# Kernel optimization log

Measured on AMD Instinct MI355X. Metric: run time of the kernel, lower is better.

## Reference

```python
import jax, jax.numpy as jnp
import numpy as np

N = 200000
E = 3200000
EPS = 1e-5


def setup_inputs() -> dict:
    key = jax.random.key(0)
    ks = jax.random.split(key, 8)
    x = jax.random.normal(ks[0], (N, 128), dtype=jnp.float32)
    edge_index = jax.random.randint(ks[1], (2, E), 0, N, dtype=jnp.int32)
    def lin(k, fi, fo):
        s = 1.0 / np.sqrt(fi)
        return jax.random.uniform(k, (fi, fo), jnp.float32, -s, s)
    return {
        "x": x,
        "edge_index": edge_index,
        "W1": lin(ks[2], 128, 256), "b1": jnp.zeros((256,), jnp.float32),
        "gamma1": jnp.ones((256,), jnp.float32), "beta1": jnp.zeros((256,), jnp.float32),
        "W2": lin(ks[3], 256, 256), "b2": jnp.zeros((256,), jnp.float32),
        "gamma2": jnp.ones((256,), jnp.float32), "beta2": jnp.zeros((256,), jnp.float32),
        "W3": lin(ks[4], 256, 40), "b3": jnp.zeros((40,), jnp.float32),
    }


def _gcn_norm(edge_index):
    # add self-loops, compute symmetric GCN normalization
    loop = jnp.arange(N, dtype=jnp.int32)
    row = jnp.concatenate([edge_index[0], loop])
    col = jnp.concatenate([edge_index[1], loop])
    deg = jax.ops.segment_sum(jnp.ones_like(row, dtype=jnp.float32), row, num_segments=N)
    dinv = jax.lax.rsqrt(jnp.maximum(deg, 1.0))  # deg >= 1 due to self-loops
    norm = dinv[row] * dinv[col]  # [E+N]
    return row, col, norm


def _gcn_conv(x, W, b, row, col, norm):
    h = x @ W                                  # [N, Fout] small GEMM
    msg = h[col] * norm[:, None]               # gather + scale  [E+N, Fout]
    out = jax.ops.segment_sum(msg, row, num_segments=N)  # scatter-add
    return out + b


def _batchnorm(x, gamma, beta):
    mu = jnp.mean(x, axis=0)
    var = jnp.var(x, axis=0)
    return (x - mu) * jax.lax.rsqrt(var + EPS) * gamma + beta


def reference(x, edge_index, W1, b1, gamma1, beta1, W2, b2, gamma2, beta2, W3, b3):
    row, col, norm = _gcn_norm(edge_index)
    h = _gcn_conv(x, W1, b1, row, col, norm)
    h = jax.nn.relu(_batchnorm(h, gamma1, beta1))
    h = _gcn_conv(h, W2, b2, row, col, norm)
    h = jax.nn.relu(_batchnorm(h, gamma2, beta2))
    h = _gcn_conv(h, W3, b3, row, col, norm)
    return jax.nn.log_softmax(h, axis=-1)
```

## Files before the change

kernel.cpp:

```cpp
#include <hip/hip_runtime.h>
#include <hip/hip_bf16.h>

#define NNODES 200000
#define NEDGES 3200000
#define NBUCK 782
#define NEB 512
#define EPB (NEDGES / NEB)
#define CASTB 12500
#define EPS 1e-5f
#define NREP 32

typedef __bf16 bf16x8 __attribute__((ext_vector_type(8)));
typedef float  f32x4  __attribute__((ext_vector_type(4)));
typedef float  f32x2  __attribute__((ext_vector_type(2)));

__device__ __forceinline__ float bflo(unsigned u) { return __uint_as_float(u << 16); }
__device__ __forceinline__ float bfhi(unsigned u) { return __uint_as_float(u & 0xffff0000u); }
__device__ __forceinline__ unsigned short f2b(float f) {
    return __builtin_bit_cast(unsigned short, __float2bfloat16(f));
}
__device__ __forceinline__ unsigned pk2(float a, float b) {
    return (unsigned)f2b(a) | ((unsigned)f2b(b) << 16);
}
__device__ __forceinline__ unsigned bnrelu_pk(unsigned u, f32x2 c, f32x2 h) {
    f32x2 v = { __uint_as_float(u << 16), __uint_as_float(u & 0xffff0000u) };
    v = __builtin_elementwise_fma(v, c, h);
    const f32x2 z = {0.f, 0.f};
    v = __builtin_elementwise_max(v, z);
    return pk2(v[0], v[1]);
}

__global__ __launch_bounds__(256) void k_cnt(const int* __restrict__ row, int* __restrict__ cnt) {
    __shared__ int h[NBUCK];
    for (int i = threadIdx.x; i < NBUCK; i += 256) h[i] = 0;
    __syncthreads();
    const int e0 = blockIdx.x * EPB;
    for (int i = e0 + threadIdx.x; i < e0 + EPB; i += 256)
        atomicAdd(&h[row[i] >> 8], 1);
    __syncthreads();
    for (int i = threadIdx.x; i < NBUCK; i += 256)
        cnt[(size_t)blockIdx.x * NBUCK + i] = h[i];
}

__global__ __launch_bounds__(256) void k_bscan(int* __restrict__ cnt, int* __restrict__ btot) {
    const int wv = (blockIdx.x * 256 + threadIdx.x) >> 6;
    const int lane = threadIdx.x & 63;
    if (wv >= NBUCK) return;
    int v[8]; int s = 0;
#pragma unroll
    for (int j = 0; j < 8; ++j) {
        v[j] = cnt[(size_t)(lane * 8 + j) * NBUCK + wv];
        s += v[j];
    }
    int excl = s;
#pragma unroll
    for (int o = 1; o < 64; o <<= 1) {
        int t = __shfl_up(excl, o);
        if (lane >= o) excl += t;
    }
    excl -= s;
    if (lane == 63) btot[wv] = excl + s;
    int base = excl;
#pragma unroll
    for (int j = 0; j < 8; ++j) {
        int t = v[j];
        cnt[(size_t)(lane * 8 + j) * NBUCK + wv] = base;
        base += t;
    }
}

__global__ __launch_bounds__(1024) void k_btscan(const int* __restrict__ btot, int* __restrict__ bbase) {
    __shared__ int s[1024];
    int t = threadIdx.x;
    int v = (t < NBUCK) ? btot[t] : 0;
    s[t] = v;
    __syncthreads();
    for (int off = 1; off < 1024; off <<= 1) {
        int u = (t >= off) ? s[t - off] : 0;
        __syncthreads();
        s[t] += u;
        __syncthreads();
    }
    if (t < NBUCK) bbase[t + 1] = s[t];
    if (t == 0) bbase[0] = 0;
}

__global__ __launch_bounds__(256) void k_place(const int* __restrict__ row, const int* __restrict__ col,
                                               const int* __restrict__ cnt, const int* __restrict__ bbase,
                                               unsigned* __restrict__ ebuf) {
    __shared__ int base[NBUCK];
    for (int i = threadIdx.x; i < NBUCK; i += 256)
        base[i] = bbase[i] + cnt[(size_t)blockIdx.x * NBUCK + i];
    __syncthreads();
    const int e0 = blockIdx.x * EPB;
    for (int i = e0 + threadIdx.x; i < e0 + EPB; i += 256) {
        int r = row[i], c = col[i];
        int p = atomicAdd(&base[r >> 8], 1);
        ebuf[p] = ((unsigned)(r & 255) << 18) | (unsigned)c;
    }
}

__global__ __launch_bounds__(256) void k_sort2(const unsigned* __restrict__ ebuf,
                                               const int* __restrict__ bbase,
                                               int* __restrict__ offs, float* __restrict__ dinv,
                                               int* __restrict__ csr) {
    __shared__ int cnt[256];
    __shared__ int sofs[256];
    __shared__ int sc[256];
    const int b = blockIdx.x;
    const int t = threadIdx.x;
    const int n0 = b * 256;
    cnt[t] = 0;
    __syncthreads();
    const int s = bbase[b], e = bbase[b + 1];
    for (int i = s + t; i < e; i += 256)
        atomicAdd(&cnt[ebuf[i] >> 18], 1);
    __syncthreads();
    const int c = cnt[t];
    sc[t] = c;
    __syncthreads();
    for (int off = 1; off < 256; off <<= 1) {
        int v = (t >= off) ? sc[t - off] : 0;
        __syncthreads();
        sc[t] += v;
        __syncthreads();
    }
    const int excl = sc[t] - c;
    sofs[t] = s + excl;
    const int n = n0 + t;
    if (n < NNODES) {
        offs[n] = s + excl;
        dinv[n] = rsqrtf((float)(c + 1));
    }
    if (b == NBUCK - 1 && t == 0) offs[NNODES] = NEDGES;
    cnt[t] = 0;
    __syncthreads();
    for (int i = s + t; i < e; i += 256) {
        unsigned v = ebuf[i];
        int nl = v >> 18;
        int rank = atomicAdd(&cnt[nl], 1);
        csr[sofs[nl] + rank] = (int)(v & 0x3FFFFu);
    }
}

__device__ __forceinline__ void prepw_one(const float* __restrict__ W,
                                          unsigned short* __restrict__ Wswz,
                                          int K, int NOUT, int t) {
    int KSTEPS = K / 32;
    int lane = t & 63;
    int ks = (t >> 6) % KSTEPS;
    int g  = (t >> 6) / KSTEPS;
    int c = lane & 15, q = lane >> 4;
    int col = g * 16 + c;
    int k0 = ks * 32 + q * 8;
    unsigned short vals[8];
#pragma unroll
    for (int j = 0; j < 8; ++j)
        vals[j] = (col < NOUT) ? f2b(W[(size_t)(k0 + j) * NOUT + col]) : (unsigned short)0;
    *(uint4*)((char*)Wswz + (size_t)t * 16) = __builtin_bit_cast(uint4, vals);
}

__global__ __launch_bounds__(256) void k_prep(const float* __restrict__ x,
                                              const float* __restrict__ dinv,
                                              uint4* __restrict__ xb,
                                              const float* __restrict__ W1,
                                              const float* __restrict__ W2,
                                              const float* __restrict__ W3,
                                              unsigned short* __restrict__ w1s,
                                              unsigned short* __restrict__ w2s,
                                              unsigned short* __restrict__ w3s) {
    const int blk = blockIdx.x;
    if (blk < CASTB) {
        size_t t = (size_t)blk * 256 + threadIdx.x;
        int n = (int)(t >> 4);
        float d = dinv[n];
        const float4* xp = (const float4*)(x + t * 8);
        float4 a = xp[0], b = xp[1];
        uint4 o;
        o.x = pk2(a.x * d, a.y * d); o.y = pk2(a.z * d, a.w * d);
        o.z = pk2(b.x * d, b.y * d); o.w = pk2(b.z * d, b.w * d);
        xb[t] = o;
    } else {
        int t = (blk - CASTB) * 256 + threadIdx.x;
        if (t < 4096) prepw_one(W1, w1s, 128, 256, t);
        else if (t < 4096 + 8192) prepw_one(W2, w2s, 256, 256, t - 4096);
        else if (t < 4096 + 8192 + 1536) prepw_one(W3, w3s, 256, 40, t - 12288);
    }
}

__global__ __launch_bounds__(256) void k_aggf(const uint4* __restrict__ in,
                                              const int* __restrict__ offs,
                                              const int* __restrict__ csr,
                                              const float* __restrict__ dinv,
                                              uint4* __restrict__ out) {
    const int lane = threadIdx.x & 63;
    const int grp = lane >> 4;
    const int fl = lane & 15;
    const int node = blockIdx.x * 4 + (threadIdx.x >> 6);
    const int p0 = offs[node];
    const int K = offs[node + 1] - p0 + 1;
    float a0=0,a1=0,a2=0,a3=0,a4=0,a5=0,a6=0,a7=0;
    auto accum = [&](uint4 u) {
        a0 += bflo(u.x); a1 += bfhi(u.x);
        a2 += bflo(u.y); a3 += bfhi(u.y);
        a4 += bflo(u.z); a5 += bfhi(u.z);
        a6 += bflo(u.w); a7 += bfhi(u.w);
    };
    int k = 0;
    for (; k + 8 <= K; k += 8) {
        int j0 = k + grp, j1 = k + 4 + grp;
        int i0 = (j0 == 0) ? node : csr[p0 + j0 - 1];
        int i1 = csr[p0 + j1 - 1];
        uint4 u0 = in[(size_t)i0 * 16 + fl];
        uint4 u1 = in[(size_t)i1 * 16 + fl];
        accum(u0); accum(u1);
    }
    for (; k + 4 <= K; k += 4) {
        int j0 = k + grp;
        int i0 = (j0 == 0) ? node : csr[p0 + j0 - 1];
        accum(in[(size_t)i0 * 16 + fl]);
    }
    int rem = K - k;
    if (grp < rem) {
        int j0 = k + grp;
        int i0 = (j0 == 0) ? node : csr[p0 + j0 - 1];
        accum(in[(size_t)i0 * 16 + fl]);
    }
#define RED(v) v += __shfl_xor(v, 32); v += __shfl_xor(v, 16);
    RED(a0) RED(a1) RED(a2) RED(a3) RED(a4) RED(a5) RED(a6) RED(a7)
#undef RED
    if (grp == 0) {
        const float d = dinv[node];
        uint4 o;
        o.x = pk2(a0 * d, a1 * d); o.y = pk2(a2 * d, a3 * d);
        o.z = pk2(a4 * d, a5 * d); o.w = pk2(a6 * d, a7 * d);
        out[(size_t)node * 16 + fl] = o;
    }
}

__global__ __launch_bounds__(256) void k_aggb(const uint4* __restrict__ in,
                                              const int* __restrict__ offs,
                                              const int* __restrict__ csr,
                                              const float* __restrict__ dinv,
                                              uint4* __restrict__ out,
                                              float* __restrict__ statr) {
    __shared__ __align__(16) float zrow[4][256];
    const int lane = threadIdx.x & 63;
    const int half = lane >> 5;
    const int fl = lane & 31;
    const int wv = threadIdx.x >> 6;
    const int node = blockIdx.x * 4 + wv;
    const int p0 = offs[node];
    const int K = offs[node + 1] - p0 + 1;
    float a0=0,a1=0,a2=0,a3=0,a4=0,a5=0,a6=0,a7=0;
    auto accum = [&](uint4 u) {
        a0 += bflo(u.x); a1 += bfhi(u.x);
        a2 += bflo(u.y); a3 += bfhi(u.y);
        a4 += bflo(u.z); a5 += bfhi(u.z);
        a6 += bflo(u.w); a7 += bfhi(u.w);
    };
    auto idxAt = [&](int j) -> int { return (j == 0) ? node : csr[p0 + j - 1]; };
    int k = 0;
    for (; k + 8 <= K; k += 8) {
        int i0 = idxAt(k + half);
        int i1 = csr[p0 + k + 1 + half];
        int i2 = csr[p0 + k + 3 + half];
        int i3 = csr[p0 + k + 5 + half];
        uint4 u0 = in[(size_t)i0 * 32 + fl];
        uint4 u1 = in[(size_t)i1 * 32 + fl];
        uint4 u2 = in[(size_t)i2 * 32 + fl];
        uint4 u3 = in[(size_t)i3 * 32 + fl];
        accum(u0); accum(u1); accum(u2); accum(u3);
    }
    for (; k + 2 <= K; k += 2) {
        accum(in[(size_t)idxAt(k + half) * 32 + fl]);
    }
    if (k < K && half == 0) {
        accum(in[(size_t)idxAt(k) * 32 + fl]);
    }
#define RED(v) v += __shfl_xor(v, 32);
    RED(a0) RED(a1) RED(a2) RED(a3) RED(a4) RED(a5) RED(a6) RED(a7)
#undef RED
    if (half == 0) {
        const float d = dinv[node];
        float v0 = a0 * d, v1 = a1 * d, v2 = a2 * d, v3 = a3 * d;
        float v4 = a4 * d, v5 = a5 * d, v6 = a6 * d, v7 = a7 * d;
        uint4 o;
        o.x = pk2(v0, v1); o.y = pk2(v2, v3);
        o.z = pk2(v4, v5); o.w = pk2(v6, v7);
        out[(size_t)node * 32 + fl] = o;
        *(float4*)&zrow[wv][fl * 8]     = float4{v0, v1, v2, v3};
        *(float4*)&zrow[wv][fl * 8 + 4] = float4{v4, v5, v6, v7};
    }
    __syncthreads();
    const int c = threadIdx.x;
    float s = 0.f, s2 = 0.f;
#pragma unroll
    for (int w = 0; w < 4; ++w) {
        float v = zrow[w][c];
        s += v; s2 += v * v;
    }
    float* rb = statr + (size_t)(blockIdx.x & (NREP - 1)) * 512;
    atomicAdd(&rb[c], s);
    atomicAdd(&rb[256 + c], s2);
}

__global__ __launch_bounds__(256) void k_agg3(const uint4* __restrict__ T3b,
                                              const int* __restrict__ offs,
                                              const int* __restrict__ csr,
                                              const float* __restrict__ dinv,
                                              const float* __restrict__ b3,
                                              float* __restrict__ out) {
    const int lane = threadIdx.x & 63;
    const int grp = lane / 5;
    const int fl = lane - grp * 5;
    const bool act = grp < 12;
    const int node = blockIdx.x * 4 + (threadIdx.x >> 6);
    const int p0 = offs[node];
    const int K = offs[node + 1] - p0 + 1;
    float a0=0,a1=0,a2=0,a3=0,a4=0,a5=0,a6=0,a7=0;
    auto accum = [&](uint4 u) {
        a0 += bflo(u.x); a1 += bfhi(u.x);
        a2 += bflo(u.y); a3 += bfhi(u.y);
        a4 += bflo(u.z); a5 += bfhi(u.z);
        a6 += bflo(u.w); a7 += bfhi(u.w);
    };
    const char* Tb = (const char*)T3b;
    int k = 0;
    if (act) {
        for (; k + 12 <= K; k += 12) {
            int j = k + grp;
            int i0 = (j == 0) ? node : csr[p0 + j - 1];
            accum(*(const uint4*)(Tb + (size_t)i0 * 80 + fl * 16));
        }
        int rem = K - k;
        if (grp < rem) {
            int j = k + grp;
            int i0 = (j == 0) ? node : csr[p0 + j - 1];
            accum(*(const uint4*)(Tb + (size_t)i0 * 80 + fl * 16));
        }
    }
#define RED3(v) { float t = __shfl(v, lane + 30); v += t; t = __shfl(v, lane + 15); v += t; \
                  float u1 = __shfl(v, lane + 5); float u2 = __shfl(v, lane + 10); v += u1 + u2; }
    RED3(a0) RED3(a1) RED3(a2) RED3(a3) RED3(a4) RED3(a5) RED3(a6) RED3(a7)
#undef RED3
    const float d = dinv[node];
    float v[8];
    if (grp == 0) {
        const float4* bp = (const float4*)(b3 + fl * 8);
        float4 b01 = bp[0], b23 = bp[1];
        v[0] = a0 * d + b01.x; v[1] = a1 * d + b01.y;
        v[2] = a2 * d + b01.z; v[3] = a3 * d + b01.w;
        v[4] = a4 * d + b23.x; v[5] = a5 * d + b23.y;
        v[6] = a6 * d + b23.z; v[7] = a7 * d + b23.w;
    } else {
#pragma unroll
        for (int j = 0; j < 8; ++j) v[j] = -INFINITY;
    }
    float m = v[0];
#pragma unroll
    for (int j = 1; j < 8; ++j) m = fmaxf(m, v[j]);
    float mm = __shfl(m, 0);
#pragma unroll
    for (int l = 1; l < 5; ++l) mm = fmaxf(mm, __shfl(m, l));
    float e = 0.f;
    if (grp == 0) {
#pragma unroll
        for (int j = 0; j < 8; ++j) e += __expf(v[j] - mm);
    }
    float s = __shfl(e, 0);
#pragma unroll
    for (int l = 1; l < 5; ++l) s += __shfl(e, l);
    float ls = __logf(s);
    if (grp == 0) {
        float* op = out + (size_t)node * 40 + fl * 8;
        float4 o0 = {v[0] - mm - ls, v[1] - mm - ls, v[2] - mm - ls, v[3] - mm - ls};
        float4 o1 = {v[4] - mm - ls, v[5] - mm - ls, v[6] - mm - ls, v[7] - mm - ls};
        *(float4*)op = o0;
        *(float4*)(op + 4) = o1;
    }
}

template <int K, int MW, int NW, int WNB, bool PRESCALE, bool BNA, bool STATS>
__global__ __launch_bounds__(MW * NW * 64) void k_gemm(const __hip_bfloat16* __restrict__ A,
                                                       const __hip_bfloat16* __restrict__ Wswz,
                                                       const float* __restrict__ dinvp,
                                                       const float* __restrict__ bnsc,
                                                       const float* __restrict__ bnsh,
                                                       unsigned short* __restrict__ Cout,
                                                       int M, int NOUT,
                                                       float* __restrict__ sums,
                                                       float* __restrict__ sq) {
    constexpr int KSTEPS = K / 32;
    const int lane = threadIdx.x & 63;
    const int wid  = threadIdx.x >> 6;
    const int wm = (wid % MW) * 64;
    const int wn = (wid / MW) * (WNB * 16);
    const long rowBase = (long)blockIdx.x * (MW * 64);
    const int cl = lane & 15, q = lane >> 4;

    const __hip_bfloat16* aptr[4];
#pragma unroll
    for (int mf = 0; mf < 4; ++mf) {
        long r = rowBase + wm + mf * 16 + cl;
        if (r > M - 1) r = M - 1;
        aptr[mf] = A + r * K + q * 8;
    }
    const __hip_bfloat16* bptr[WNB];
#pragma unroll
    for (int nf = 0; nf < WNB; ++nf) {
        int g = wn / 16 + nf;
        bptr[nf] = Wswz + (size_t)g * KSTEPS * 512 + (size_t)lane * 8;
    }

    f32x4 acc[4][WNB];
    const f32x4 z = {0.f, 0.f, 0.f, 0.f};
#pragma unroll
    for (int mf = 0; mf < 4; ++mf)
#pragma unroll
        for (int nf = 0; nf < WNB; ++nf) acc[mf][nf] = z;

#pragma unroll
    for (int ks = 0; ks < KSTEPS; ++ks) {
        f32x2 cp0, cp1, cp2, cp3, hp0, hp1, hp2, hp3;
        if constexpr (BNA) {
            const int k0 = ks * 32 + q * 8;
            const f32x2* cp = (const f32x2*)(bnsc + k0);
            const f32x2* hp = (const f32x2*)(bnsh + k0);
            cp0 = cp[0]; cp1 = cp[1]; cp2 = cp[2]; cp3 = cp[3];
            hp0 = hp[0]; hp1 = hp[1]; hp2 = hp[2]; hp3 = hp[3];
        }
        bf16x8 a[4], b[WNB];
#pragma unroll
        for (int mf = 0; mf < 4; ++mf) {
            uint4 u = *(const uint4*)(aptr[mf] + ks * 32);
            if constexpr (BNA) {
                uint4 o;
                o.x = bnrelu_pk(u.x, cp0, hp0);
                o.y = bnrelu_pk(u.y, cp1, hp1);
                o.z = bnrelu_pk(u.z, cp2, hp2);
                o.w = bnrelu_pk(u.w, cp3, hp3);
                u = o;
            }
            a[mf] = __builtin_bit_cast(bf16x8, u);
        }
#pragma unroll
        for (int nf = 0; nf < WNB; ++nf)
            b[nf] = __builtin_bit_cast(bf16x8, *(const uint4*)(bptr[nf] + ks * 512));
#pragma unroll
        for (int mf = 0; mf < 4; ++mf)
#pragma unroll
            for (int nf = 0; nf < WNB; ++nf)
                acc[mf][nf] = __builtin_amdgcn_mfma_f32_16x16x32_bf16(a[mf], b[nf], acc[mf][nf], 0, 0, 0);
    }

#pragma unroll
    for (int mf = 0; mf < 4; ++mf)
#pragma unroll
        for (int i = 0; i < 4; ++i) {
            long row = rowBase + wm + mf * 16 + q * 4 + i;
            if (row >= M) continue;
            float dv = PRESCALE ? dinvp[row] : 1.0f;
#pragma unroll
            for (int nf = 0; nf < WNB; ++nf) {
                int col = wn + nf * 16 + cl;
                if (col < NOUT)
                    Cout[row * NOUT + col] = f2b(PRESCALE ? acc[mf][nf][i] * dv : acc[mf][nf][i]);
            }
        }

    if constexpr (STATS) {
#pragma unroll
        for (int nf = 0; nf < WNB; ++nf) {
            float s = 0.f, s2 = 0.f;
#pragma unroll
            for (int mf = 0; mf < 4; ++mf)
#pragma unroll
                for (int i = 0; i < 4; ++i) {
                    long row = rowBase + wm + mf * 16 + q * 4 + i;
                    float v = (row < M) ? acc[mf][nf][i] : 0.f;
                    s += v; s2 += v * v;
                }
            s  += __shfl_xor(s, 16);  s  += __shfl_xor(s, 32);
            s2 += __shfl_xor(s2, 16); s2 += __shfl_xor(s2, 32);
            if (q == 0) {
                int col = wn + nf * 16 + cl;
                if (col < NOUT) {
                    atomicAdd(&sums[col], s);
                    atomicAdd(&sq[col], s2);
                }
            }
        }
    }
}

__global__ __launch_bounds__(256) void k_bnfin(const float* __restrict__ sums,
                                               const float* __restrict__ sq,
                                               const float* __restrict__ gamma,
                                               const float* __restrict__ beta,
                                               float* __restrict__ scale,
                                               float* __restrict__ shift) {
    const int t = threadIdx.x;
    float mu = sums[t] * (1.0f / NNODES);
    float var = sq[t] * (1.0f / NNODES) - mu * mu;
    if (var < 0.f) var = 0.f;
    float sc = gamma[t] * rsqrtf(var + EPS);
    scale[t] = sc;
    shift[t] = beta[t] - mu * sc;
}

__global__ __launch_bounds__(256) void k_bnfin2(const float* __restrict__ statr,
                                                const float* __restrict__ gamma,
                                                const float* __restrict__ beta,
                                                float* __restrict__ scale,
                                                float* __restrict__ shift) {
    const int t = threadIdx.x;
    float s = 0.f, s2 = 0.f;
#pragma unroll
    for (int r = 0; r < NREP; ++r) {
        s  += statr[(size_t)r * 512 + t];
        s2 += statr[(size_t)r * 512 + 256 + t];
    }
    float mu = s * (1.0f / NNODES);
    float var = s2 * (1.0f / NNODES) - mu * mu;
    if (var < 0.f) var = 0.f;
    float sc = gamma[t] * rsqrtf(var + EPS);
    scale[t] = sc;
    shift[t] = beta[t] - mu * sc;
}

extern "C" void kernel_launch(void* const* d_in, const int* in_sizes, int n_in,
                              void* d_out, int out_size, void* d_ws, size_t ws_size,
                              hipStream_t stream) {
    const float* x   = (const float*)d_in[0];
    const int*   ei  = (const int*)d_in[1];
    const float* W1  = (const float*)d_in[2];
    const float* g1  = (const float*)d_in[4];
    const float* be1 = (const float*)d_in[5];
    const float* W2  = (const float*)d_in[6];
    const float* g2  = (const float*)d_in[8];
    const float* be2 = (const float*)d_in[9];
    const float* W3  = (const float*)d_in[10];
    const float* b3  = (const float*)d_in[11];

    char* w = (char*)d_ws;
    size_t o = 0;
    auto alloc = [&](size_t b) { size_t r = o; o += (b + 255) & ~(size_t)255; return r; };
    int*   offs = (int*)(w + alloc((size_t)(NNODES + 1) * 4));
    float* dinv = (float*)(w + alloc((size_t)NNODES * 4));
    int*   cnt  = (int*)(w + alloc((size_t)NEB * NBUCK * 4));
    int*   btot = (int*)(w + alloc(NBUCK * 4));
    int*   bbase= (int*)(w + alloc((NBUCK + 1) * 4));
    unsigned* ebuf = (unsigned*)(w + alloc((size_t)NEDGES * 4));
    int*   csr  = (int*)(w + alloc((size_t)NEDGES * 4));
    float* stats = (float*)(w + alloc((512 + NREP * 512) * 4));
    float* bnp   = (float*)(w + alloc(4 * 256 * 4));
    unsigned short* w1s = (unsigned short*)(w + alloc(65536));
    unsigned short* w2s = (unsigned short*)(w + alloc(131072));
    unsigned short* w3s = (unsigned short*)(w + alloc(24576));
    __hip_bfloat16* xb   = (__hip_bfloat16*)(w + alloc((size_t)NNODES * 128 * 2));
    __hip_bfloat16* buf0 = (__hip_bfloat16*)(w + alloc((size_t)NNODES * 128 * 2));
    __hip_bfloat16* buf1 = (__hip_bfloat16*)(w + alloc((size_t)NNODES * 256 * 2));
    __hip_bfloat16* buf2 = (__hip_bfloat16*)(w + alloc((size_t)NNODES * 256 * 2));

    float* sums1 = stats;       float* sq1 = stats + 256;
    float* statr = stats + 512;
    float* scale1 = bnp;        float* shift1 = bnp + 256;
    float* scale2 = bnp + 512;  float* shift2 = bnp + 768;

    hipMemsetAsync(stats, 0, (512 + NREP * 512) * 4, stream);

    k_cnt<<<NEB, 256, 0, stream>>>(ei, cnt);
    k_bscan<<<(NBUCK * 64 + 255) / 256, 256, 0, stream>>>(cnt, btot);
    k_btscan<<<1, 1024, 0, stream>>>(btot, bbase);
    k_place<<<NEB, 256, 0, stream>>>(ei, ei + NEDGES, cnt, bbase, ebuf);
    k_sort2<<<NBUCK, 256, 0, stream>>>(ebuf, bbase, offs, dinv, csr);
    k_prep<<<CASTB + 54, 256, 0, stream>>>(x, dinv, (uint4*)xb, W1, W2, W3, w1s, w2s, w3s);

    const dim3 g64((NNODES + 63) / 64, 1);

    k_aggf<<<NNODES / 4, 256, 0, stream>>>((const uint4*)xb, offs, csr, dinv, (uint4*)buf0);
    k_gemm<128, 1, 4, 4, false, false, true><<<g64, 256, 0, stream>>>(buf0, (const __hip_bfloat16*)w1s, nullptr, nullptr, nullptr, (unsigned short*)buf1, NNODES, 256, sums1, sq1);
    k_bnfin<<<1, 256, 0, stream>>>(sums1, sq1, g1, be1, scale1, shift1);

    k_gemm<256, 1, 4, 4, true, true, false><<<g64, 256, 0, stream>>>(buf1, (const __hip_bfloat16*)w2s, dinv, scale1, shift1, (unsigned short*)buf2, NNODES, 256, nullptr, nullptr);
    k_aggb<<<NNODES / 4, 256, 0, stream>>>((const uint4*)buf2, offs, csr, dinv, (uint4*)buf1, statr);
    k_bnfin2<<<1, 256, 0, stream>>>(statr, g2, be2, scale2, shift2);

    k_gemm<256, 4, 1, 3, true, true, false><<<dim3((NNODES + 255) / 256, 1), 256, 0, stream>>>(buf1, (const __hip_bfloat16*)w3s, dinv, scale2, shift2, (unsigned short*)buf0, NNODES, 40, nullptr, nullptr);
    k_agg3<<<NNODES / 4, 256, 0, stream>>>((const uint4*)buf0, offs, csr, dinv, b3, (float*)d_out);
}
```

Measured before the change: 1.056 ms.

## Persistent-grid aggb with register stats; pad layer-3 rows to 128 bytes

k_aggb becomes a grid-stride kernel with 2048 blocks. Each lane keeps per-feature sum and sum-of-squares in registers across its nodes, then issues one set of atomics at the end, which replaces the per-block shared-memory reduction, __syncthreads and 512 atomics per block. Layer-3 GEMM output rows are padded from 80 to 128 bytes through a new row-stride parameter, so the gathers in k_agg3 are cache-line aligned. The cost is fewer blocks to hide gather latency in aggb and a larger layer-3 buffer footprint.

```diff
diff --git a/kernel.cpp b/kernel.cpp
--- a/kernel.cpp
+++ b/kernel.cpp
@@ -8,7 +8,9 @@
 #define EPB (NEDGES / NEB)
 #define CASTB 12500
 #define EPS 1e-5f
-#define NREP 32
+#define NQUAD (NNODES / 4)
+#define AGGB_BLOCKS 2048
+#define NREP2 16
 
 typedef __bf16 bf16x8 __attribute__((ext_vector_type(8)));
 typedef float  f32x4  __attribute__((ext_vector_type(4)));
@@ -244,65 +246,69 @@
                                               const float* __restrict__ dinv,
                                               uint4* __restrict__ out,
                                               float* __restrict__ statr) {
-    __shared__ __align__(16) float zrow[4][256];
     const int lane = threadIdx.x & 63;
     const int half = lane >> 5;
     const int fl = lane & 31;
     const int wv = threadIdx.x >> 6;
-    const int node = blockIdx.x * 4 + wv;
-    const int p0 = offs[node];
-    const int K = offs[node + 1] - p0 + 1;
-    float a0=0,a1=0,a2=0,a3=0,a4=0,a5=0,a6=0,a7=0;
-    auto accum = [&](uint4 u) {
-        a0 += bflo(u.x); a1 += bfhi(u.x);
-        a2 += bflo(u.y); a3 += bfhi(u.y);
-        a4 += bflo(u.z); a5 += bfhi(u.z);
-        a6 += bflo(u.w); a7 += bfhi(u.w);
-    };
-    auto idxAt = [&](int j) -> int { return (j == 0) ? node : csr[p0 + j - 1]; };
-    int k = 0;
-    for (; k + 8 <= K; k += 8) {
-        int i0 = idxAt(k + half);
-        int i1 = csr[p0 + k + 1 + half];
-        int i2 = csr[p0 + k + 3 + half];
-        int i3 = csr[p0 + k + 5 + half];
-        uint4 u0 = in[(size_t)i0 * 32 + fl];
-        uint4 u1 = in[(size_t)i1 * 32 + fl];
-        uint4 u2 = in[(size_t)i2 * 32 + fl];
-        uint4 u3 = in[(size_t)i3 * 32 + fl];
-        accum(u0); accum(u1); accum(u2); accum(u3);
-    }
-    for (; k + 2 <= K; k += 2) {
-        accum(in[(size_t)idxAt(k + half) * 32 + fl]);
-    }
-    if (k < K && half == 0) {
-        accum(in[(size_t)idxAt(k) * 32 + fl]);
-    }
+    float s[8], s2[8];
+#pragma unroll
+    for (int j = 0; j < 8; ++j) { s[j] = 0.f; s2[j] = 0.f; }
+
+    for (int bq = blockIdx.x; bq < NQUAD; bq += AGGB_BLOCKS) {
+        const int node = bq * 4 + wv;
+        const int p0 = offs[node];
+        const int K = offs[node + 1] - p0 + 1;
+        float a0=0,a1=0,a2=0,a3=0,a4=0,a5=0,a6=0,a7=0;
+        auto accum = [&](uint4 u) {
+            a0 += bflo(u.x); a1 += bfhi(u.x);
+            a2 += bflo(u.y); a3 += bfhi(u.y);
+            a4 += bflo(u.z); a5 += bfhi(u.z);
+            a6 += bflo(u.w); a7 += bfhi(u.w);
+        };
+        auto idxAt = [&](int j) -> int { return (j == 0) ? node : csr[p0 + j - 1]; };
+        int k = 0;
+        for (; k + 8 <= K; k += 8) {
+            int i0 = idxAt(k + half);
+            int i1 = csr[p0 + k + 1 + half];
+            int i2 = csr[p0 + k + 3 + half];
+            int i3 = csr[p0 + k + 5 + half];
+            uint4 u0 = in[(size_t)i0 * 32 + fl];
+            uint4 u1 = in[(size_t)i1 * 32 + fl];
+            uint4 u2 = in[(size_t)i2 * 32 + fl];
+            uint4 u3 = in[(size_t)i3 * 32 + fl];
+            accum(u0); accum(u1); accum(u2); accum(u3);
+        }
+        for (; k + 2 <= K; k += 2) {
+            accum(in[(size_t)idxAt(k + half) * 32 + fl]);
+        }
+        if (k < K && half == 0) {
+            accum(in[(size_t)idxAt(k) * 32 + fl]);
+        }
 #define RED(v) v += __shfl_xor(v, 32);
-    RED(a0) RED(a1) RED(a2) RED(a3) RED(a4) RED(a5) RED(a6) RED(a7)
+        RED(a0) RED(a1) RED(a2) RED(a3) RED(a4) RED(a5) RED(a6) RED(a7)
 #undef RED
+        if (half == 0) {
+            const float d = dinv[node];
+            float v0 = a0 * d, v1 = a1 * d, v2 = a2 * d, v3 = a3 * d;
+            float v4 = a4 * d, v5 = a5 * d, v6 = a6 * d, v7 = a7 * d;
+            uint4 o;
+            o.x = pk2(v0, v1); o.y = pk2(v2, v3);
+            o.z = pk2(v4, v5); o.w = pk2(v6, v7);
+            out[(size_t)node * 32 + fl] = o;
+            s[0] += v0; s2[0] += v0 * v0;  s[1] += v1; s2[1] += v1 * v1;
+            s[2] += v2; s2[2] += v2 * v2;  s[3] += v3; s2[3] += v3 * v3;
+            s[4] += v4; s2[4] += v4 * v4;  s[5] += v5; s2[5] += v5 * v5;
+            s[6] += v6; s2[6] += v6 * v6;  s[7] += v7; s2[7] += v7 * v7;
+        }
+    }
     if (half == 0) {
-        const float d = dinv[node];
-        float v0 = a0 * d, v1 = a1 * d, v2 = a2 * d, v3 = a3 * d;
-        float v4 = a4 * d, v5 = a5 * d, v6 = a6 * d, v7 = a7 * d;
-        uint4 o;
-        o.x = pk2(v0, v1); o.y = pk2(v2, v3);
-        o.z = pk2(v4, v5); o.w = pk2(v6, v7);
-        out[(size_t)node * 32 + fl] = o;
-        *(float4*)&zrow[wv][fl * 8]     = float4{v0, v1, v2, v3};
-        *(float4*)&zrow[wv][fl * 8 + 4] = float4{v4, v5, v6, v7};
-    }
-    __syncthreads();
-    const int c = threadIdx.x;
-    float s = 0.f, s2 = 0.f;
-#pragma unroll
-    for (int w = 0; w < 4; ++w) {
-        float v = zrow[w][c];
-        s += v; s2 += v * v;
-    }
-    float* rb = statr + (size_t)(blockIdx.x & (NREP - 1)) * 512;
-    atomicAdd(&rb[c], s);
-    atomicAdd(&rb[256 + c], s2);
+        float* rb = statr + (size_t)(blockIdx.x & (NREP2 - 1)) * 512;
+#pragma unroll
+        for (int j = 0; j < 8; ++j) {
+            atomicAdd(&rb[fl * 8 + j], s[j]);
+            atomicAdd(&rb[256 + fl * 8 + j], s2[j]);
+        }
+    }
 }
 
 __global__ __launch_bounds__(256) void k_agg3(const uint4* __restrict__ T3b,
@@ -331,13 +337,13 @@
         for (; k + 12 <= K; k += 12) {
             int j = k + grp;
             int i0 = (j == 0) ? node : csr[p0 + j - 1];
-            accum(*(const uint4*)(Tb + (size_t)i0 * 80 + fl * 16));
+            accum(*(const uint4*)(Tb + (size_t)i0 * 128 + fl * 16));
         }
         int rem = K - k;
         if (grp < rem) {
             int j = k + grp;
             int i0 = (j == 0) ? node : csr[p0 + j - 1];
-            accum(*(const uint4*)(Tb + (size_t)i0 * 80 + fl * 16));
+            accum(*(const uint4*)(Tb + (size_t)i0 * 128 + fl * 16));
         }
     }
 #define RED3(v) { float t = __shfl(v, lane + 30); v += t; t = __shfl(v, lane + 15); v += t; \
@@ -388,7 +394,7 @@
                                                        const float* __restrict__ bnsc,
                                                        const float* __restrict__ bnsh,
                                                        unsigned short* __restrict__ Cout,
-                                                       int M, int NOUT,
+                                                       int M, int NOUT, int CS,
                                                        float* __restrict__ sums,
                                                        float* __restrict__ sq) {
     constexpr int KSTEPS = K / 32;
@@ -465,7 +471,7 @@
             for (int nf = 0; nf < WNB; ++nf) {
                 int col = wn + nf * 16 + cl;
                 if (col < NOUT)
-                    Cout[row * NOUT + col] = f2b(PRESCALE ? acc[mf][nf][i] * dv : acc[mf][nf][i]);
+                    Cout[row * CS + col] = f2b(PRESCALE ? acc[mf][nf][i] * dv : acc[mf][nf][i]);
             }
         }
 
@@ -517,7 +523,7 @@
     const int t = threadIdx.x;
     float s = 0.f, s2 = 0.f;
 #pragma unroll
-    for (int r = 0; r < NREP; ++r) {
+    for (int r = 0; r < NREP2; ++r) {
         s  += statr[(size_t)r * 512 + t];
         s2 += statr[(size_t)r * 512 + 256 + t];
     }
@@ -553,7 +559,7 @@
     int*   bbase= (int*)(w + alloc((NBUCK + 1) * 4));
     unsigned* ebuf = (unsigned*)(w + alloc((size_t)NEDGES * 4));
     int*   csr  = (int*)(w + alloc((size_t)NEDGES * 4));
-    float* stats = (float*)(w + alloc((512 + NREP * 512) * 4));
+    float* stats = (float*)(w + alloc((512 + NREP2 * 512) * 4));
     float* bnp   = (float*)(w + alloc(4 * 256 * 4));
     unsigned short* w1s = (unsigned short*)(w + alloc(65536));
     unsigned short* w2s = (unsigned short*)(w + alloc(131072));
@@ -568,7 +574,7 @@
     float* scale1 = bnp;        float* shift1 = bnp + 256;
     float* scale2 = bnp + 512;  float* shift2 = bnp + 768;
 
-    hipMemsetAsync(stats, 0, (512 + NREP * 512) * 4, stream);
+    hipMemsetAsync(stats, 0, (512 + NREP2 * 512) * 4, stream);
 
     k_cnt<<<NEB, 256, 0, stream>>>(ei, cnt);
     k_bscan<<<(NBUCK * 64 + 255) / 256, 256, 0, stream>>>(cnt, btot);
@@ -580,13 +586,13 @@
     const dim3 g64((NNODES + 63) / 64, 1);
 
     k_aggf<<<NNODES / 4, 256, 0, stream>>>((const uint4*)xb, offs, csr, dinv, (uint4*)buf0);
-    k_gemm<128, 1, 4, 4, false, false, true><<<g64, 256, 0, stream>>>(buf0, (const __hip_bfloat16*)w1s, nullptr, nullptr, nullptr, (unsigned short*)buf1, NNODES, 256, sums1, sq1);
+    k_gemm<128, 1, 4, 4, false, false, true><<<g64, 256, 0, stream>>>(buf0, (const __hip_bfloat16*)w1s, nullptr, nullptr, nullptr, (unsigned short*)buf1, NNODES, 256, 256, sums1, sq1);
     k_bnfin<<<1, 256, 0, stream>>>(sums1, sq1, g1, be1, scale1, shift1);
 
-    k_gemm<256, 1, 4, 4, true, true, false><<<g64, 256, 0, stream>>>(buf1, (const __hip_bfloat16*)w2s, dinv, scale1, shift1, (unsigned short*)buf2, NNODES, 256, nullptr, nullptr);
-    k_aggb<<<NNODES / 4, 256, 0, stream>>>((const uint4*)buf2, offs, csr, dinv, (uint4*)buf1, statr);
+    k_gemm<256, 1, 4, 4, true, true, false><<<g64, 256, 0, stream>>>(buf1, (const __hip_bfloat16*)w2s, dinv, scale1, shift1, (unsigned short*)buf2, NNODES, 256, 256, nullptr, nullptr);
+    k_aggb<<<AGGB_BLOCKS, 256, 0, stream>>>((const uint4*)buf2, offs, csr, dinv, (uint4*)buf1, statr);
     k_bnfin2<<<1, 256, 0, stream>>>(statr, g2, be2, scale2, shift2);
 
-    k_gemm<256, 4, 1, 3, true, true, false><<<dim3((NNODES + 255) / 256, 1), 256, 0, stream>>>(buf1, (const __hip_bfloat16*)w3s, dinv, scale2, shift2, (unsigned short*)buf0, NNODES, 40, nullptr, nullptr);
+    k_gemm<256, 4, 1, 3, true, true, false><<<dim3((NNODES + 255) / 256, 1), 256, 0, stream>>>(buf1, (const __hip_bfloat16*)w3s, dinv, scale2, shift2, (unsigned short*)buf0, NNODES, 40, 64, nullptr, nullptr);
     k_agg3<<<NNODES / 4, 256, 0, stream>>>((const uint4*)buf0, offs, csr, dinv, b3, (float*)d_out);
 }
```

Result: slower. 1.293 ms (+22.5%).
